# Optimization experiments

Measured on AMD Instinct MI355X. Metric: run time of the kernel, lower is better.

The kernel has to match this reference:

```python
import jax, jax.numpy as jnp
import numpy as np

H, KV, D = 16, 4, 128
WIN = 512
EPS = 1e-6


def rms_norm(x, w):
    # x: [..., D]
    return x * jax.lax.rsqrt(jnp.mean(x * x, axis=-1, keepdims=True) + EPS) * w


def rotate_half(x):
    x1, x2 = jnp.split(x, 2, axis=-1)
    return jnp.concatenate([-x2, x1], axis=-1)


def setup_inputs() -> dict:
    key = jax.random.key(0)
    ks = jax.random.split(key, 8)
    B, L, hidden = 2, 2048, 2048
    x = jax.random.normal(ks[0], (B, L, hidden), jnp.float32)
    # realistic RoPE tables
    inv_freq = 1.0 / (10000.0 ** (np.arange(0, D, 2, dtype=np.float32) / D))
    t = np.arange(L, dtype=np.float32)
    freqs = np.outer(t, inv_freq)  # [L, D/2]
    emb = np.concatenate([freqs, freqs], axis=-1)  # [L, D]
    cos = jnp.asarray(np.cos(emb), jnp.float32)
    sin = jnp.asarray(np.sin(emb), jnp.float32)
    s = 0.02
    Wq = jax.random.normal(ks[1], (H * D, hidden), jnp.float32) * s
    Wk = jax.random.normal(ks[2], (KV * D, hidden), jnp.float32) * s
    Wv = jax.random.normal(ks[3], (KV * D, hidden), jnp.float32) * s
    Wo = jax.random.normal(ks[4], (hidden, H * D), jnp.float32) * s
    q_norm_w = jnp.ones((D,), jnp.float32)
    k_norm_w = jnp.ones((D,), jnp.float32)
    return {"x": x, "cos": cos, "sin": sin, "Wq": Wq, "Wk": Wk, "Wv": Wv,
            "Wo": Wo, "q_norm_w": q_norm_w, "k_norm_w": k_norm_w}


def reference(x, cos, sin, Wq, Wk, Wv, Wo, q_norm_w, k_norm_w):
    B, L, _ = x.shape
    # projections (torch Linear: y = x @ W.T)
    q = (x @ Wq.T).reshape(B, L, H, D)
    k = (x @ Wk.T).reshape(B, L, KV, D)
    v = (x @ Wv.T).reshape(B, L, KV, D)
    # QK RMSNorm, then [B, heads, L, D]
    q = jnp.transpose(rms_norm(q, q_norm_w), (0, 2, 1, 3))
    k = jnp.transpose(rms_norm(k, k_norm_w), (0, 2, 1, 3))
    v = jnp.transpose(v, (0, 2, 1, 3))
    # RoPE
    c = cos[None, None]  # [1,1,L,D]
    s = sin[None, None]
    q = q * c + rotate_half(q) * s
    k = k * c + rotate_half(k) * s
    # GQA repeat_interleave over head dim
    n_rep = H // KV
    k = jnp.repeat(k, n_rep, axis=1)
    v = jnp.repeat(v, n_rep, axis=1)
    # sliding-window additive bias [L, L]
    idx = jnp.arange(L)
    in_win = jnp.abs(idx[:, None] - idx[None, :]) <= WIN
    bias = jnp.where(in_win, 0.0, jnp.finfo(x.dtype).min).astype(x.dtype)
    # SDPA
    scale = 1.0 / jnp.sqrt(jnp.asarray(D, x.dtype))
    scores = jnp.einsum('bhqd,bhkd->bhqk', q, k) * scale + bias[None, None]
    attn = jax.nn.softmax(scores, axis=-1)
    out = jnp.einsum('bhqk,bhkd->bhqd', attn, v)  # [B,H,L,D]
    out = jnp.transpose(out, (0, 2, 1, 3)).reshape(B, L, H * D)
    return out @ Wo.T
```

## Files before the change

kernel.cpp:

```cpp
#include <hip/hip_runtime.h>
#include <hip/hip_bf16.h>


typedef unsigned short u16;
typedef unsigned int u32;
typedef __attribute__((ext_vector_type(8))) short bf16x8;
typedef __attribute__((ext_vector_type(4))) float f32x4;

#define AS1 __attribute__((address_space(1)))
#define AS3 __attribute__((address_space(3)))

__device__ __forceinline__ u16 f2b(float f) {
  union { float f; u32 u; } c; c.f = f;
  return (u16)((c.u + 0x8000u) >> 16);
}
__device__ __forceinline__ float b2f(u16 u) {
  union { u32 u; float f; } c; c.u = ((u32)u) << 16; return c.f;
}

__global__ __launch_bounds__(256) void cvt_all(const float* __restrict__ x,
                                               const float* __restrict__ wq,
                                               const float* __restrict__ wk,
                                               const float* __restrict__ wv,
                                               const float* __restrict__ wo,
                                               u16* __restrict__ xb,
                                               u16* __restrict__ wqkvb,
                                               u16* __restrict__ wob) {
  int blk = blockIdx.x;
  const float* s; u16* d; int off;
  if (blk < 8192)       { s = x;  d = xb;              off = blk * 1024; }
  else if (blk < 12288) { s = wq; d = wqkvb;           off = (blk - 8192) * 1024; }
  else if (blk < 13312) { s = wk; d = wqkvb + 4194304; off = (blk - 12288) * 1024; }
  else if (blk < 14336) { s = wv; d = wqkvb + 5242880; off = (blk - 13312) * 1024; }
  else                  { s = wo; d = wob;             off = (blk - 14336) * 1024; }
  int i = off + threadIdx.x * 4;
  float4 v = *(const float4*)(s + i);
  ushort4 o;
  o.x = f2b(v.x); o.y = f2b(v.y); o.z = f2b(v.z); o.w = f2b(v.w);
  *(ushort4*)(d + i) = o;
}

template<int F32OUT>
__global__ __launch_bounds__(256) void gemm_bt(const u16* __restrict__ A,
                                               const u16* __restrict__ Bm,
                                               void* __restrict__ C,
                                               int M, int N, int K) {
  __shared__ u16 As[128][64];
  __shared__ u16 Bs[128][64];
  const int tid  = threadIdx.x;
  const int w    = tid >> 6, lane = tid & 63, quad = lane >> 4, l16 = lane & 15;
  const int wm   = w >> 1, wn = w & 1;
  const int m0   = blockIdx.y * 128, n0 = blockIdx.x * 128;

  f32x4 zero = {0.f, 0.f, 0.f, 0.f};
  f32x4 acc[4][4];
#pragma unroll
  for (int i = 0; i < 4; i++)
#pragma unroll
    for (int j = 0; j < 4; j++) acc[i][j] = zero;

  const int srow = lane >> 3;
  const int swz8 = ((lane & 7) ^ (lane >> 3)) * 8;

  for (int k0 = 0; k0 < K; k0 += 64) {
#pragma unroll
    for (int p = 0; p < 4; ++p) {
      int row = p * 32 + w * 8 + srow;
      __builtin_amdgcn_global_load_lds(
          (const AS1 void*)(A + (size_t)(m0 + row) * K + k0 + swz8),
          (AS3 void*)((char*)&As[0][0] + p * 4096 + w * 1024), 16, 0, 0);
      __builtin_amdgcn_global_load_lds(
          (const AS1 void*)(Bm + (size_t)(n0 + row) * K + k0 + swz8),
          (AS3 void*)((char*)&Bs[0][0] + p * 4096 + w * 1024), 16, 0, 0);
    }
    __syncthreads();
#pragma unroll
    for (int kk = 0; kk < 64; kk += 32) {
      const int cs = ((kk >> 3) + quad) ^ (l16 & 7);
      bf16x8 af[4], bfr[4];
#pragma unroll
      for (int i = 0; i < 4; i++)
        af[i] = *(const bf16x8*)((const char*)&As[0][0] +
                                 (wm * 64 + i * 16 + l16) * 128 + cs * 16);
#pragma unroll
      for (int j = 0; j < 4; j++)
        bfr[j] = *(const bf16x8*)((const char*)&Bs[0][0] +
                                  (wn * 64 + j * 16 + l16) * 128 + cs * 16);
#pragma unroll
      for (int i = 0; i < 4; i++)
#pragma unroll
        for (int j = 0; j < 4; j++)
          acc[i][j] = __builtin_amdgcn_mfma_f32_16x16x32_bf16(af[i], bfr[j], acc[i][j], 0, 0, 0);
    }
    __syncthreads();
  }

#pragma unroll
  for (int i = 0; i < 4; i++) {
#pragma unroll
    for (int r = 0; r < 4; r++) {
      int gr = m0 + wm * 64 + i * 16 + quad * 4 + r;
#pragma unroll
      for (int j = 0; j < 4; j++) {
        int gc = n0 + wn * 64 + j * 16 + l16;
        if (F32OUT) ((float*)C)[(size_t)gr * N + gc] = acc[i][j][r];
        else        ((u16*)C)[(size_t)gr * N + gc]   = f2b(acc[i][j][r]);
      }
    }
  }
}

__global__ __launch_bounds__(256) void rmsrope(const u16* __restrict__ qkv,
                                               const float* __restrict__ cosT,
                                               const float* __restrict__ sinT,
                                               const float* __restrict__ qw,
                                               const float* __restrict__ kw,
                                               u16* __restrict__ qo,
                                               u16* __restrict__ ko) {
  int wid  = blockIdx.x * 4 + (threadIdx.x >> 6);
  int lane = threadIdx.x & 63;
  int r  = wid / 20;
  int hh = wid % 20;
  int b = r >> 11, l = r & 2047;
  int cb = hh < 16 ? hh * 128 : 2048 + (hh - 16) * 128;
  const u16* src = qkv + (size_t)r * 3072 + cb;
  float v0 = b2f(src[lane]);
  float v1 = b2f(src[lane + 64]);
  float ss = v0 * v0 + v1 * v1;
#pragma unroll
  for (int off = 1; off < 64; off <<= 1) ss += __shfl_xor(ss, off, 64);
  float inv = rsqrtf(ss * (1.0f / 128.0f) + 1e-6f);
  const float* wt = hh < 16 ? qw : kw;
  float n0 = v0 * inv * wt[lane];
  float n1 = v1 * inv * wt[lane + 64];
  float c0 = cosT[l * 128 + lane],      c1 = cosT[l * 128 + 64 + lane];
  float s0 = sinT[l * 128 + lane],      s1 = sinT[l * 128 + 64 + lane];
  float o0 = n0 * c0 - n1 * s0;
  float o1 = n1 * c1 + n0 * s1;
  const float qscale = 0.08838834764831845f * 1.4426950408889634f;
  u16* dst; size_t base;
  if (hh < 16) { dst = qo; base = ((size_t)(b * 16 + hh) * 2048 + l) * 128;
                 o0 *= qscale; o1 *= qscale; }
  else         { dst = ko; base = ((size_t)(b * 4 + (hh - 16)) * 2048 + l) * 128; }
  dst[base + lane]      = f2b(o0);
  dst[base + 64 + lane] = f2b(o1);
}

__global__ __launch_bounds__(256) void transpose_v(const u16* __restrict__ qkv,
                                                   u16* __restrict__ dst) {
  __shared__ u16 T[64][72];
  const int lt = blockIdx.x, dt = blockIdx.y, bh = blockIdx.z;
  const int b = bh >> 2, kv = bh & 3;
  const u16* s = qkv + ((size_t)(b * 2048 + lt * 64)) * 3072 + 2560 + kv * 128 + dt * 64;
  u16*       d = dst + (size_t)bh * 128 * 2048 + (size_t)dt * 64 * 2048 + lt * 64;
  const int t = threadIdx.x;
  const int row = t >> 3, c8 = (t & 7) * 8;
#pragma unroll
  for (int p = 0; p < 2; ++p)
    *(uint4*)&T[p * 32 + row][c8] = *(const uint4*)(s + (size_t)(p * 32 + row) * 3072 + c8);
  __syncthreads();
#pragma unroll
  for (int p = 0; p < 2; ++p) {
    int dr = p * 32 + row;
    u16 o[8];
#pragma unroll
    for (int j = 0; j < 8; ++j) o[j] = T[c8 + j][dr];
    *(uint4*)(d + (size_t)dr * 2048 + c8) = *(uint4*)o;
  }
}

__global__ __launch_bounds__(256) void flash_swa(const u16* __restrict__ Q,
                                                 const u16* __restrict__ Kg,
                                                 const u16* __restrict__ VTg,
                                                 u16* __restrict__ Og) {
  constexpr int L = 2048, D = 128;
  __shared__ u16 Ks[64][136];
  __shared__ u16 Vt[128][72];
  __shared__ u16 Ps[4][16][72];

  const int q0  = blockIdx.x * 64;
  const int h   = blockIdx.y;
  const int b   = blockIdx.z;
  const int tid = threadIdx.x;
  const int w = tid >> 6, lane = tid & 63, quad = lane >> 4, l16 = lane & 15;
  const int kvh = h >> 2;

  const u16* Qb  = Q   + (size_t)(b * 16 + h)  * L * D;
  const u16* Kb  = Kg  + (size_t)(b * 4 + kvh) * L * D;
  const u16* VTb = VTg + (size_t)(b * 4 + kvh) * D * L;

  bf16x8 qf[4];
  {
    int qr = q0 + w * 16 + l16;
#pragma unroll
    for (int ks = 0; ks < 4; ++ks)
      qf[ks] = *(const bf16x8*)(Qb + (size_t)qr * D + ks * 32 + quad * 8);
  }
  const int qi = q0 + w * 16 + l16;

  f32x4 zero = {0.f, 0.f, 0.f, 0.f};
  f32x4 o[8];
#pragma unroll
  for (int i = 0; i < 8; i++) o[i] = zero;
  float lrow = 0.f;

  int kt0   = q0 > 512 ? q0 - 512 : 0;
  int ktend = q0 + 64 + 512; if (ktend > L) ktend = L;

  for (int kt = kt0; kt < ktend; kt += 64) {
#pragma unroll
    for (int p = 0; p < 4; ++p) {
      int c = tid + p * 256;
      int row = c >> 4, c8 = (c & 15) * 8;
      *(uint4*)&Ks[row][c8] = *(const uint4*)(Kb + (size_t)(kt + row) * D + c8);
    }
#pragma unroll
    for (int p = 0; p < 4; ++p) {
      int c = tid + p * 256;
      int row = c >> 3, c8 = (c & 7) * 8;
      *(uint4*)&Vt[row][c8] = *(const uint4*)(VTb + (size_t)row * L + kt + c8);
    }
    __syncthreads();

    f32x4 s[4];
#pragma unroll
    for (int ct = 0; ct < 4; ct++) s[ct] = zero;
#pragma unroll
    for (int ks = 0; ks < 4; ++ks) {
#pragma unroll
      for (int ct = 0; ct < 4; ++ct) {
        bf16x8 kf = *(const bf16x8*)&Ks[ct * 16 + l16][ks * 32 + quad * 8];
        s[ct] = __builtin_amdgcn_mfma_f32_16x16x32_bf16(kf, qf[ks], s[ct], 0, 0, 0);
      }
    }

    bool need_mask = (kt + 448 < q0) || (kt > q0 + 448);
    float psum = 0.f;
#pragma unroll
    for (int ct = 0; ct < 4; ct++) {
      u16 ph[4];
#pragma unroll
      for (int r = 0; r < 4; r++) {
        float x = s[ct][r];
        if (need_mask) {
          int ki = kt + ct * 16 + quad * 4 + r;
          int dd = qi - ki; if (dd < 0) dd = -dd;
          if (dd > 512) x = -__builtin_inff();
        }
        float p = exp2f(x);
        psum += p;
        ph[r] = f2b(p);
      }
      uint2 pk;
      pk.x = (u32)ph[0] | ((u32)ph[1] << 16);
      pk.y = (u32)ph[2] | ((u32)ph[3] << 16);
      *(uint2*)&Ps[w][l16][ct * 16 + quad * 4] = pk;
    }
    psum += __shfl_xor(psum, 16, 64);
    psum += __shfl_xor(psum, 32, 64);
    lrow += psum;

    bf16x8 pf[2];
#pragma unroll
    for (int ks2 = 0; ks2 < 2; ++ks2)
      pf[ks2] = *(const bf16x8*)&Ps[w][l16][ks2 * 32 + quad * 8];
#pragma unroll
    for (int dt = 0; dt < 8; ++dt) {
#pragma unroll
      for (int ks2 = 0; ks2 < 2; ++ks2) {
        bf16x8 vf = *(const bf16x8*)&Vt[dt * 16 + l16][ks2 * 32 + quad * 8];
        o[dt] = __builtin_amdgcn_mfma_f32_16x16x32_bf16(pf[ks2], vf, o[dt], 0, 0, 0);
      }
    }
    __syncthreads();
  }

#pragma unroll
  for (int r = 0; r < 4; r++) {
    float lv  = __shfl(lrow, (lane & 48) + quad * 4 + r, 64);
    float inv = 1.0f / lv;
    int qr = q0 + w * 16 + quad * 4 + r;
    size_t base = ((size_t)(b * L + qr)) * 2048 + h * 128;
#pragma unroll
    for (int dt = 0; dt < 8; dt++)
      Og[base + dt * 16 + l16] = f2b(o[dt][r] * inv);
  }
}

extern "C" void kernel_launch(void* const* d_in, const int* in_sizes, int n_in,
                              void* d_out, int out_size, void* d_ws, size_t ws_size,
                              hipStream_t stream) {
  const float* x    = (const float*)d_in[0];
  const float* cosT = (const float*)d_in[1];
  const float* sinT = (const float*)d_in[2];
  const float* Wq   = (const float*)d_in[3];
  const float* Wk   = (const float*)d_in[4];
  const float* Wv   = (const float*)d_in[5];
  const float* Wo   = (const float*)d_in[6];
  const float* qw   = (const float*)d_in[7];
  const float* kw   = (const float*)d_in[8];

  char* ws = (char*)d_ws;
  u16* x_bf    = (u16*)(ws + 0);
  u16* wqkv_bf = (u16*)(ws + 16777216);
  u16* wo_bf   = (u16*)(ws + 29360128);
  u16* qkv_bf  = (u16*)(ws + 37748736);
  u16* q_bf    = (u16*)(ws + 62914560);
  u16* k_bf    = (u16*)(ws + 79691776);
  u16* vt_bf   = wqkv_bf;
  u16* attn_bf = x_bf;

  cvt_all<<<18432, 256, 0, stream>>>(x, Wq, Wk, Wv, Wo, x_bf, wqkv_bf, wo_bf);
  gemm_bt<0><<<dim3(24, 32), 256, 0, stream>>>(x_bf, wqkv_bf, qkv_bf, 4096, 3072, 2048);
  rmsrope<<<20480, 256, 0, stream>>>(qkv_bf, cosT, sinT, qw, kw, q_bf, k_bf);
  transpose_v<<<dim3(32, 2, 8), 256, 0, stream>>>(qkv_bf, vt_bf);
  flash_swa<<<dim3(32, 16, 2), 256, 0, stream>>>(q_bf, k_bf, vt_bf, attn_bf);
  gemm_bt<1><<<dim3(16, 32), 256, 0, stream>>>(attn_bf, wo_bf, d_out, 4096, 2048, 2048);
}
```

Before: 309.0 us.

## Double-buffer K/V tiles via direct global-to-LDS loads with XOR swizzle

The flash attention kernel now double-buffers its K and V^T shared-memory tiles, using global_load_lds to prefetch the next tile while the current one is computed. Padded LDS arrays are replaced by XOR-swizzled layouts for K, V and P to avoid bank conflicts without padding. s_setprio is raised around the MFMA sections. This aims to hide global load latency behind compute, at the cost of doubled LDS use and possibly lower occupancy. Only one barrier per iteration remains, so correctness relies on the async LDS writes being complete at that barrier.

Measured after the change: 315.4 us. 2.1% more time.

```diff
diff --git a/kernel.cpp b/kernel.cpp
--- a/kernel.cpp
+++ b/kernel.cpp
@@ -174,9 +174,9 @@
                                                  const u16* __restrict__ VTg,
                                                  u16* __restrict__ Og) {
   constexpr int L = 2048, D = 128;
-  __shared__ u16 Ks[64][136];
-  __shared__ u16 Vt[128][72];
-  __shared__ u16 Ps[4][16][72];
+  __shared__ u16 Ks[2][64][128];
+  __shared__ u16 Vt[2][128][64];
+  __shared__ u16 Ps[4][16][64];
 
   const int q0  = blockIdx.x * 64;
   const int h   = blockIdx.y;
@@ -198,44 +198,76 @@
   }
   const int qi = q0 + w * 16 + l16;
 
+  int kt0   = q0 > 512 ? q0 - 512 : 0;
+  int ktend = q0 + 64 + 512; if (ktend > L) ktend = L;
+  const int nt = (ktend - kt0) >> 6;
+
+  const u16* srcK[4];
+  const u16* srcV[4];
+#pragma unroll
+  for (int p = 0; p < 4; ++p) {
+    int rk = w * 16 + p * 4 + (lane >> 4);
+    int ck = ((lane & 15) ^ (rk & 7)) * 8;
+    srcK[p] = Kb + (size_t)(kt0 + rk) * D + ck;
+    int rv = w * 32 + p * 8 + (lane >> 3);
+    int cv = ((lane & 7) ^ (rv & 7)) * 8;
+    srcV[p] = VTb + (size_t)rv * L + kt0 + cv;
+  }
+
+#define STAGE(bb) do {                                                        \
+    char* kdst = (char*)&Ks[bb][0][0] + w * 4096;                             \
+    char* vdst = (char*)&Vt[bb][0][0] + w * 4096;                             \
+    _Pragma("unroll")                                                         \
+    for (int p = 0; p < 4; ++p) {                                             \
+      __builtin_amdgcn_global_load_lds((const AS1 void*)srcK[p],              \
+          (AS3 void*)(kdst + p * 1024), 16, 0, 0);                            \
+      srcK[p] += 64 * D;                                                      \
+    }                                                                         \
+    _Pragma("unroll")                                                         \
+    for (int p = 0; p < 4; ++p) {                                             \
+      __builtin_amdgcn_global_load_lds((const AS1 void*)srcV[p],              \
+          (AS3 void*)(vdst + p * 1024), 16, 0, 0);                            \
+      srcV[p] += 64;                                                          \
+    }                                                                         \
+  } while (0)
+
   f32x4 zero = {0.f, 0.f, 0.f, 0.f};
   f32x4 o[8];
 #pragma unroll
   for (int i = 0; i < 8; i++) o[i] = zero;
   float lrow = 0.f;
 
-  int kt0   = q0 > 512 ? q0 - 512 : 0;
-  int ktend = q0 + 64 + 512; if (ktend > L) ktend = L;
-
-  for (int kt = kt0; kt < ktend; kt += 64) {
-#pragma unroll
-    for (int p = 0; p < 4; ++p) {
-      int c = tid + p * 256;
-      int row = c >> 4, c8 = (c & 15) * 8;
-      *(uint4*)&Ks[row][c8] = *(const uint4*)(Kb + (size_t)(kt + row) * D + c8);
-    }
-#pragma unroll
-    for (int p = 0; p < 4; ++p) {
-      int c = tid + p * 256;
-      int row = c >> 3, c8 = (c & 7) * 8;
-      *(uint4*)&Vt[row][c8] = *(const uint4*)(VTb + (size_t)row * L + kt + c8);
-    }
-    __syncthreads();
+  STAGE(0);
+  __syncthreads();
+  int cur = 0;
+
+  const int swz = (l16 & 7) << 4;
+
+  for (int t = 0; t < nt; ++t) {
+    const int kt = kt0 + t * 64;
+    if (t + 1 < nt) STAGE(cur ^ 1);
+
+    const char* kbase = (const char*)&Ks[cur][0][0];
+    const char* vbase = (const char*)&Vt[cur][0][0];
 
     f32x4 s[4];
 #pragma unroll
     for (int ct = 0; ct < 4; ct++) s[ct] = zero;
+    __builtin_amdgcn_s_setprio(1);
 #pragma unroll
     for (int ks = 0; ks < 4; ++ks) {
 #pragma unroll
       for (int ct = 0; ct < 4; ++ct) {
-        bf16x8 kf = *(const bf16x8*)&Ks[ct * 16 + l16][ks * 32 + quad * 8];
+        bf16x8 kf = *(const bf16x8*)(kbase + (ct * 16 + l16) * 256 +
+                                     (((ks * 4 + quad) ^ (l16 & 7)) * 16));
         s[ct] = __builtin_amdgcn_mfma_f32_16x16x32_bf16(kf, qf[ks], s[ct], 0, 0, 0);
       }
     }
+    __builtin_amdgcn_s_setprio(0);
 
     bool need_mask = (kt + 448 < q0) || (kt > q0 + 448);
     float psum = 0.f;
+    char* psw = (char*)&Ps[w][l16][0];
 #pragma unroll
     for (int ct = 0; ct < 4; ct++) {
       u16 ph[4];
@@ -254,7 +286,7 @@
       uint2 pk;
       pk.x = (u32)ph[0] | ((u32)ph[1] << 16);
       pk.y = (u32)ph[2] | ((u32)ph[3] << 16);
-      *(uint2*)&Ps[w][l16][ct * 16 + quad * 4] = pk;
+      *(uint2*)(psw + ((ct * 32 + quad * 8) ^ swz)) = pk;
     }
     psum += __shfl_xor(psum, 16, 64);
     psum += __shfl_xor(psum, 32, 64);
@@ -263,17 +295,23 @@
     bf16x8 pf[2];
 #pragma unroll
     for (int ks2 = 0; ks2 < 2; ++ks2)
-      pf[ks2] = *(const bf16x8*)&Ps[w][l16][ks2 * 32 + quad * 8];
+      pf[ks2] = *(const bf16x8*)(psw + ((ks2 * 64 + quad * 16) ^ swz));
+    __builtin_amdgcn_s_setprio(1);
 #pragma unroll
     for (int dt = 0; dt < 8; ++dt) {
 #pragma unroll
       for (int ks2 = 0; ks2 < 2; ++ks2) {
-        bf16x8 vf = *(const bf16x8*)&Vt[dt * 16 + l16][ks2 * 32 + quad * 8];
+        bf16x8 vf = *(const bf16x8*)(vbase + (dt * 16 + l16) * 128 +
+                                     (((ks2 * 4 + quad) ^ (l16 & 7)) * 16));
         o[dt] = __builtin_amdgcn_mfma_f32_16x16x32_bf16(pf[ks2], vf, o[dt], 0, 0, 0);
       }
     }
+    __builtin_amdgcn_s_setprio(0);
+
     __syncthreads();
-  }
+    cur ^= 1;
+  }
+#undef STAGE
 
 #pragma unroll
   for (int r = 0; r < 4; r++) {
```
